# Kernel optimization log

Hardware: AMD Instinct MI355X
Metric: run time of the kernel (lower is better)

The kernel has to match this reference:

```python
import jax, jax.numpy as jnp
import numpy as np

N_NODES = 200000  # num_users + num_items
N_EDGES = 500000
LATENT = 64
N_LAYERS = 3
NEG_SLOPE = 0.01  # F.leaky_relu default
EPS = 1e-16       # PyG geo_softmax denominator epsilon


def setup_inputs() -> dict:
    key = jax.random.key(0)
    k1, k2, k3, k4, k5 = jax.random.split(key, 5)
    edge_index = jax.random.randint(k1, (2, N_EDGES), 0, N_NODES, dtype=jnp.int64 if jax.config.jax_enable_x64 else jnp.int32)
    edge_attrs = jax.random.normal(k2, (N_EDGES, 2), dtype=jnp.float32)
    emb = jax.random.normal(k3, (N_NODES, LATENT), dtype=jnp.float32)
    # per-layer attention params, shape [L, heads=1 -> squeezed, in_channels]
    a_att_w = jax.random.normal(k4, (N_LAYERS, LATENT), dtype=jnp.float32) * 0.1
    r_att_w = jax.random.normal(k5, (N_LAYERS, LATENT), dtype=jnp.float32) * 0.1
    return {"edge_index": edge_index, "edge_attrs": edge_attrs, "emb": emb,
            "a_att_w": a_att_w, "r_att_w": r_att_w}


def _segment_softmax(scores, dst, num_nodes):
    # scores: [E, D] softmax over edges grouped by destination node (PyG geo_softmax)
    m = jax.ops.segment_max(scores, dst, num_segments=num_nodes)  # [N, D]
    m = jnp.where(jnp.isfinite(m), m, 0.0)  # nodes without incoming edges
    w = jnp.exp(scores - m[dst])
    den = jax.ops.segment_sum(w, dst, num_segments=num_nodes)     # [N, D]
    return w / (den[dst] + EPS)


def reference(edge_index, edge_attrs, emb, a_att_w, r_att_w):
    src, dst = edge_index[0], edge_index[1]
    n = emb.shape[0]
    # symmetric degree normalization (degree of destination endpoints)
    deg = jax.ops.segment_sum(jnp.ones_like(dst, dtype=emb.dtype), dst, num_segments=n)
    dinv = jnp.where(deg > 0, deg ** -0.5, 0.0)
    norm = (dinv[src] * dinv[dst])[:, None]  # [E, 1]

    a_e = edge_attrs[:, 0:1]  # [E, 1]
    r_e = edge_attrs[:, 1:2]

    x = emb
    acc = emb  # layer-0 embedding
    for l in range(N_LAYERS):
        scores = (jax.nn.leaky_relu(a_e * a_att_w[l], NEG_SLOPE)
                  + jax.nn.leaky_relu(r_e * r_att_w[l], NEG_SLOPE))  # [E, D]
        attn = _segment_softmax(scores, dst, n)                       # [E, D]
        msg = norm * attn * x[src]                                    # gather + weight
        x = jax.ops.segment_sum(msg, dst, num_segments=n)             # scatter-add
        acc = acc + x
    out = acc / (N_LAYERS + 1)  # mean over layer embeddings
    return out
```

## Files before the change

kernel.cpp:

```cpp
#include <hip/hip_runtime.h>

#define BLK 256
#define LBLK 256
#define CH 1024

__device__ __forceinline__ unsigned short f2bf(float f) {
    unsigned u = __float_as_uint(f);
    u += 0x7FFFu + ((u >> 16) & 1u);
    return (unsigned short)(u >> 16);
}
__device__ __forceinline__ float bf2f(unsigned short h) {
    return __uint_as_float((unsigned)h << 16);
}
__device__ __forceinline__ float4 unpack4(ushort4 h) {
    return make_float4(bf2f(h.x), bf2f(h.y), bf2f(h.z), bf2f(h.w));
}
__device__ __forceinline__ ushort4 pack4(float4 f) {
    ushort4 h; h.x = f2bf(f.x); h.y = f2bf(f.y); h.z = f2bf(f.z); h.w = f2bf(f.w);
    return h;
}


__global__ void k_deg(const int* __restrict__ dst, int* __restrict__ deg,
                      int* __restrict__ rank, int E) {
    int e = blockIdx.x * blockDim.x + threadIdx.x;
    if (e < E) rank[e] = atomicAdd(&deg[dst[e]], 1);
}

__global__ void k_scan1(const int* __restrict__ deg, int* __restrict__ partials, int N) {
    __shared__ int sm[BLK];
    int i0 = blockIdx.x * CH + threadIdx.x * 4;
    int s = 0;
    if (i0 + 3 < N) {
        int4 v = *(const int4*)(deg + i0);
        s = (v.x + v.y) + (v.z + v.w);
    } else {
        for (int k = 0; k < 4; ++k) if (i0 + k < N) s += deg[i0 + k];
    }
    sm[threadIdx.x] = s;
    __syncthreads();
    for (int off = BLK / 2; off > 0; off >>= 1) {
        if (threadIdx.x < off) sm[threadIdx.x] += sm[threadIdx.x + off];
        __syncthreads();
    }
    if (threadIdx.x == 0) partials[blockIdx.x] = sm[0];
}

__global__ void k_scan2(const int* __restrict__ deg, const int* __restrict__ partials,
                        int* __restrict__ row_off, int N, int E, int nb) {
    __shared__ int sp[BLK];
    __shared__ int sm[BLK];
    int b = blockIdx.x, t = threadIdx.x;
    sp[t] = (t < nb) ? partials[t] : 0;
    __syncthreads();
    for (int off = 1; off < BLK; off <<= 1) {
        int add = (t >= off) ? sp[t - off] : 0;
        __syncthreads();
        sp[t] += add;
        __syncthreads();
    }
    int base = (b == 0) ? 0 : sp[b - 1];
    if (b == 0 && t == 0) row_off[N] = E;
    int i0 = b * CH + t * 4;
    int v0 = 0, v1 = 0, v2 = 0, v3 = 0;
    if (i0 + 3 < N) {
        int4 v = *(const int4*)(deg + i0);
        v0 = v.x; v1 = v.y; v2 = v.z; v3 = v.w;
    } else {
        if (i0     < N) v0 = deg[i0];
        if (i0 + 1 < N) v1 = deg[i0 + 1];
        if (i0 + 2 < N) v2 = deg[i0 + 2];
    }
    int tot = (v0 + v1) + (v2 + v3);
    sm[t] = tot;
    __syncthreads();
    for (int off = 1; off < BLK; off <<= 1) {
        int add = (t >= off) ? sm[t - off] : 0;
        __syncthreads();
        sm[t] += add;
        __syncthreads();
    }
    int excl = base + sm[t] - tot;
    int4 r;
    r.x = excl;
    r.y = excl + v0;
    r.z = excl + v0 + v1;
    r.w = excl + v0 + v1 + v2;
    if (i0 + 3 < N) {
        *(int4*)(row_off + i0) = r;
    } else {
        if (i0     < N) row_off[i0]     = r.x;
        if (i0 + 1 < N) row_off[i0 + 1] = r.y;
        if (i0 + 2 < N) row_off[i0 + 2] = r.z;
    }
}

__global__ void k_convfill(const int* __restrict__ src, const int* __restrict__ dst,
                           const float2* __restrict__ attrs, const int* __restrict__ row_off,
                           const int* __restrict__ rank, const int* __restrict__ deg,
                           uint2* __restrict__ csr, const float4* __restrict__ emb4,
                           ushort4* __restrict__ embs, int E, int N16, int gF) {
    int b = blockIdx.x;
    if (b < gF) {
        int e = b * BLK + threadIdx.x;
        if (e >= E) return;
        int pos = row_off[dst[e]] + rank[e];
        float2 ar = attrs[e];
        csr[pos] = make_uint2((unsigned)src[e],
                              (unsigned)f2bf(ar.x) | ((unsigned)f2bf(ar.y) << 16));
    } else {
        int i = (b - gF) * BLK + threadIdx.x;
        if (i >= N16) return;
        int d = deg[i >> 4];
        float dinv = (d > 0) ? rsqrtf((float)d) : 0.0f;
        float4 e = emb4[i];
        embs[i] = pack4(make_float4(dinv * e.x, dinv * e.y, dinv * e.z, dinv * e.w));
    }
}


__device__ __forceinline__ float lrelu(float x) { return fmaxf(x, 0.01f * x); }

__device__ __forceinline__ float4 edge_w4(unsigned ar, const float4& aw, const float4& rw) {
    float a = bf2f((unsigned short)(ar & 0xffffu));
    float r = bf2f((unsigned short)(ar >> 16));
    float4 w;
    w.x = __expf(lrelu(a * aw.x) + lrelu(r * rw.x));
    w.y = __expf(lrelu(a * aw.y) + lrelu(r * rw.y));
    w.z = __expf(lrelu(a * aw.z) + lrelu(r * rw.z));
    w.w = __expf(lrelu(a * aw.w) + lrelu(r * rw.w));
    return w;
}

__device__ __forceinline__ void acc4(float4& num, float4& den,
                                     const float4& w, const ushort4& h, float g) {
    float4 x = unpack4(h);
    den.x += g * w.x; den.y += g * w.y; den.z += g * w.z; den.w += g * w.w;
    num.x += g * w.x * x.x;
    num.y += g * w.y * x.y;
    num.z += g * w.z * x.z;
    num.w += g * w.w * x.w;
}

template<int MODE>
__global__ __launch_bounds__(LBLK) void k_layer(
    const ushort4* __restrict__ xs, const uint2* __restrict__ csr,
    const int* __restrict__ row_off,
    const float4* __restrict__ aw4, const float4* __restrict__ rw4,
    const float4* __restrict__ emb4,
    const ushort4* __restrict__ xsA, const ushort4* __restrict__ xsB,
    ushort4* __restrict__ xsout, float4* __restrict__ out4, int N) {
    const int t = threadIdx.x;
    const int d4 = t & 15;
    const int v = blockIdx.x * (LBLK / 16) + (t >> 4);
    if (v >= N) return;
    const float4 aw = aw4[d4];
    const float4 rw = rw4[d4];
    const int s0 = row_off[v];
    const int s1 = row_off[v + 1];
    const int dv = s1 - s0;
    float4 num = {0.f, 0.f, 0.f, 0.f};
    float4 den = {0.f, 0.f, 0.f, 0.f};
    for (int i = s0; i < s1; i += 4) {
        const int last = s1 - 1;
        uint2 e0 = csr[i];
        uint2 e1 = csr[min(i + 1, last)];
        uint2 e2 = csr[min(i + 2, last)];
        uint2 e3 = csr[min(i + 3, last)];
        ushort4 h0 = xs[(size_t)e0.x * 16 + d4];
        ushort4 h1 = xs[(size_t)e1.x * 16 + d4];
        ushort4 h2 = xs[(size_t)e2.x * 16 + d4];
        ushort4 h3 = xs[(size_t)e3.x * 16 + d4];
        float4 w0 = edge_w4(e0.y, aw, rw);
        float4 w1 = edge_w4(e1.y, aw, rw);
        float4 w2 = edge_w4(e2.y, aw, rw);
        float4 w3 = edge_w4(e3.y, aw, rw);
        float g1 = (i + 1 < s1) ? 1.0f : 0.0f;
        float g2 = (i + 2 < s1) ? 1.0f : 0.0f;
        float g3 = (i + 3 < s1) ? 1.0f : 0.0f;
        acc4(num, den, w0, h0, 1.0f);
        acc4(num, den, w1, h1, g1);
        acc4(num, den, w2, h2, g2);
        acc4(num, den, w3, h3, g3);
    }
    float4 xr;
    xr.x = num.x / (den.x + 1e-16f);
    xr.y = num.y / (den.y + 1e-16f);
    xr.z = num.z / (den.z + 1e-16f);
    xr.w = num.w / (den.w + 1e-16f);
    const float dinv = (dv > 0) ? rsqrtf((float)dv) : 0.0f;
    const size_t o = (size_t)v * 16 + d4;
    if (MODE == 2) {
        const float sd = (dv > 0) ? sqrtf((float)dv) : 0.0f;
        float4 e = emb4[o];
        float4 A = unpack4(xsA[o]);
        float4 B = unpack4(xsB[o]);
        float4 r;
        r.x = (e.x + sd * (A.x + B.x) + dinv * xr.x) * 0.25f;
        r.y = (e.y + sd * (A.y + B.y) + dinv * xr.y) * 0.25f;
        r.z = (e.z + sd * (A.z + B.z) + dinv * xr.z) * 0.25f;
        r.w = (e.w + sd * (A.w + B.w) + dinv * xr.w) * 0.25f;
        out4[o] = r;
    } else {
        const float s = dinv * dinv;
        xsout[o] = pack4(make_float4(s * xr.x, s * xr.y, s * xr.z, s * xr.w));
    }
}


extern "C" void kernel_launch(void* const* d_in, const int* in_sizes, int n_in,
                              void* d_out, int out_size, void* d_ws, size_t ws_size,
                              hipStream_t stream) {
    const int*   ei    = (const int*)d_in[0];
    const float* attrs = (const float*)d_in[1];
    const float* emb   = (const float*)d_in[2];
    const float* a_att = (const float*)d_in[3];
    const float* r_att = (const float*)d_in[4];

    const int E = in_sizes[0] / 2;
    const int N = in_sizes[2] / 64;
    const int* src = ei;
    const int* dst = ei + E;

    char* ws = (char*)d_ws;
    size_t off = 0;
    auto alloc = [&](size_t bytes) {
        void* p = ws + off;
        off += (bytes + 255) & ~(size_t)255;
        return p;
    };
    int*     deg      = (int*)alloc((size_t)N * 4);
    int*     rank     = (int*)alloc((size_t)E * 4);
    int*     row_off  = (int*)alloc((size_t)(N + 1) * 4);
    int*     partials = (int*)alloc((size_t)BLK * 4);
    uint2*   csr      = (uint2*)alloc((size_t)E * 8);
    ushort4* embs     = (ushort4*)alloc((size_t)N * 16 * 8);
    ushort4* xsA      = (ushort4*)alloc((size_t)N * 16 * 8);
    ushort4* xsB      = (ushort4*)alloc((size_t)N * 16 * 8);
    float4*  out      = (float4*)d_out;

    hipMemsetAsync(deg, 0, (size_t)N * 4, stream);

    int gE = (E + BLK - 1) / BLK;
    int nb = (N + CH - 1) / CH;
    int gF = gE;
    int gC = (N * 16 + BLK - 1) / BLK;

    k_deg     <<<gE, BLK, 0, stream>>>(dst, deg, rank, E);
    k_scan1   <<<nb, BLK, 0, stream>>>(deg, partials, N);
    k_scan2   <<<nb, BLK, 0, stream>>>(deg, partials, row_off, N, E, nb);
    k_convfill<<<gF + gC, BLK, 0, stream>>>(src, dst, (const float2*)attrs, row_off,
                                            rank, deg, csr, (const float4*)emb,
                                            embs, E, N * 16, gF);

    const float4* emb4 = (const float4*)emb;
    const float4* aw4  = (const float4*)a_att;
    const float4* rw4  = (const float4*)r_att;

    int gL = (N + (LBLK / 16) - 1) / (LBLK / 16);
    k_layer<0><<<gL, LBLK, 0, stream>>>(embs, csr, row_off, aw4,      rw4,
                                        nullptr, nullptr, nullptr, xsA, nullptr, N);
    k_layer<1><<<gL, LBLK, 0, stream>>>(xsA,  csr, row_off, aw4 + 16, rw4 + 16,
                                        nullptr, nullptr, nullptr, xsB, nullptr, N);
    k_layer<2><<<gL, LBLK, 0, stream>>>(xsB,  csr, row_off, aw4 + 32, rw4 + 32,
                                        emb4, xsA, xsB, nullptr, out, N);
}
```

Measured before the change: 239.3 us.

## Add per-node first-four-edge table to break the row_off to CSR dependency chain

The fill kernel also writes each node's first four edge records into a fixed-stride table, zeroed by an extra memset. The layer kernel reads that table directly by node id, so it can issue the first four neighbour gathers at once instead of waiting for row_off and then the CSR loads. Edges 5 to 8 are prefetched early and the MODE 2 epilogue loads are hoisted. This costs an extra 6.4MB table write plus a memset, and more registers.

```diff
diff --git a/kernel.cpp b/kernel.cpp
--- a/kernel.cpp
+++ b/kernel.cpp
@@ -98,21 +98,25 @@
 __global__ void k_convfill(const int* __restrict__ src, const int* __restrict__ dst,
                            const float2* __restrict__ attrs, const int* __restrict__ row_off,
                            const int* __restrict__ rank, const int* __restrict__ deg,
-                           uint2* __restrict__ csr, const float4* __restrict__ emb4,
+                           uint2* __restrict__ csr, uint2* __restrict__ f4,
+                           const float4* __restrict__ emb4,
                            ushort4* __restrict__ embs, int E, int N16, int gF) {
     int b = blockIdx.x;
     if (b < gF) {
         int e = b * BLK + threadIdx.x;
         if (e >= E) return;
-        int pos = row_off[dst[e]] + rank[e];
+        int d  = dst[e];
+        int rk = rank[e];
         float2 ar = attrs[e];
-        csr[pos] = make_uint2((unsigned)src[e],
-                              (unsigned)f2bf(ar.x) | ((unsigned)f2bf(ar.y) << 16));
+        uint2 rec = make_uint2((unsigned)src[e],
+                               (unsigned)f2bf(ar.x) | ((unsigned)f2bf(ar.y) << 16));
+        csr[row_off[d] + rk] = rec;
+        if (rk < 4) f4[(size_t)d * 4 + rk] = rec;
     } else {
         int i = (b - gF) * BLK + threadIdx.x;
         if (i >= N16) return;
-        int d = deg[i >> 4];
-        float dinv = (d > 0) ? rsqrtf((float)d) : 0.0f;
+        int dg = deg[i >> 4];
+        float dinv = (dg > 0) ? rsqrtf((float)dg) : 0.0f;
         float4 e = emb4[i];
         embs[i] = pack4(make_float4(dinv * e.x, dinv * e.y, dinv * e.z, dinv * e.w));
     }
@@ -145,7 +149,7 @@
 template<int MODE>
 __global__ __launch_bounds__(LBLK) void k_layer(
     const ushort4* __restrict__ xs, const uint2* __restrict__ csr,
-    const int* __restrict__ row_off,
+    const uint2* __restrict__ f4, const int* __restrict__ row_off,
     const float4* __restrict__ aw4, const float4* __restrict__ rw4,
     const float4* __restrict__ emb4,
     const ushort4* __restrict__ xsA, const ushort4* __restrict__ xsB,
@@ -154,52 +158,121 @@
     const int d4 = t & 15;
     const int v = blockIdx.x * (LBLK / 16) + (t >> 4);
     if (v >= N) return;
+    const unsigned nm1 = (unsigned)(N - 1);
+    const size_t o = (size_t)v * 16 + d4;
+
     const float4 aw = aw4[d4];
     const float4 rw = rw4[d4];
+
+    const uint4 fa = *(const uint4*)(f4 + (size_t)v * 4);
+    const uint4 fb = *(const uint4*)(f4 + (size_t)v * 4 + 2);
     const int s0 = row_off[v];
     const int s1 = row_off[v + 1];
-    const int dv = s1 - s0;
+
+    float4 emb_v = {0,0,0,0}, Av = {0,0,0,0}, Bv = {0,0,0,0};
+    if (MODE == 2) {
+        emb_v = emb4[o];
+        Av = unpack4(xsA[o]);
+        Bv = unpack4(xsB[o]);
+    }
+
+    ushort4 h0 = xs[(size_t)min(fa.x, nm1) * 16 + d4];
+    ushort4 h1 = xs[(size_t)min(fa.z, nm1) * 16 + d4];
+    ushort4 h2 = xs[(size_t)min(fb.x, nm1) * 16 + d4];
+    ushort4 h3 = xs[(size_t)min(fb.z, nm1) * 16 + d4];
+
     float4 num = {0.f, 0.f, 0.f, 0.f};
     float4 den = {0.f, 0.f, 0.f, 0.f};
-    for (int i = s0; i < s1; i += 4) {
-        const int last = s1 - 1;
-        uint2 e0 = csr[i];
-        uint2 e1 = csr[min(i + 1, last)];
-        uint2 e2 = csr[min(i + 2, last)];
-        uint2 e3 = csr[min(i + 3, last)];
-        ushort4 h0 = xs[(size_t)e0.x * 16 + d4];
-        ushort4 h1 = xs[(size_t)e1.x * 16 + d4];
-        ushort4 h2 = xs[(size_t)e2.x * 16 + d4];
-        ushort4 h3 = xs[(size_t)e3.x * 16 + d4];
-        float4 w0 = edge_w4(e0.y, aw, rw);
-        float4 w1 = edge_w4(e1.y, aw, rw);
-        float4 w2 = edge_w4(e2.y, aw, rw);
-        float4 w3 = edge_w4(e3.y, aw, rw);
-        float g1 = (i + 1 < s1) ? 1.0f : 0.0f;
-        float g2 = (i + 2 < s1) ? 1.0f : 0.0f;
-        float g3 = (i + 3 < s1) ? 1.0f : 0.0f;
-        acc4(num, den, w0, h0, 1.0f);
+
+    if (s0 + 4 < s1) {
+        const int l = max(s1 - 1, 0);
+        uint2 e4 = csr[min(s0 + 4, l)];
+        uint2 e5 = csr[min(s0 + 5, l)];
+        uint2 e6 = csr[min(s0 + 6, l)];
+        uint2 e7 = csr[min(s0 + 7, l)];
+        ushort4 h4 = xs[(size_t)min(e4.x, nm1) * 16 + d4];
+        ushort4 h5 = xs[(size_t)min(e5.x, nm1) * 16 + d4];
+        ushort4 h6 = xs[(size_t)min(e6.x, nm1) * 16 + d4];
+        ushort4 h7 = xs[(size_t)min(e7.x, nm1) * 16 + d4];
+        {
+            const float g0 = (s0     < s1) ? 1.0f : 0.0f;
+            const float g1 = (s0 + 1 < s1) ? 1.0f : 0.0f;
+            const float g2 = (s0 + 2 < s1) ? 1.0f : 0.0f;
+            const float g3 = (s0 + 3 < s1) ? 1.0f : 0.0f;
+            float4 w0 = edge_w4(fa.y, aw, rw);
+            float4 w1 = edge_w4(fa.w, aw, rw);
+            float4 w2 = edge_w4(fb.y, aw, rw);
+            float4 w3 = edge_w4(fb.w, aw, rw);
+            acc4(num, den, w0, h0, g0);
+            acc4(num, den, w1, h1, g1);
+            acc4(num, den, w2, h2, g2);
+            acc4(num, den, w3, h3, g3);
+        }
+        {
+            const float g4 = (s0 + 4 < s1) ? 1.0f : 0.0f;
+            const float g5 = (s0 + 5 < s1) ? 1.0f : 0.0f;
+            const float g6 = (s0 + 6 < s1) ? 1.0f : 0.0f;
+            const float g7 = (s0 + 7 < s1) ? 1.0f : 0.0f;
+            float4 w4 = edge_w4(e4.y, aw, rw);
+            float4 w5 = edge_w4(e5.y, aw, rw);
+            float4 w6 = edge_w4(e6.y, aw, rw);
+            float4 w7 = edge_w4(e7.y, aw, rw);
+            acc4(num, den, w4, h4, g4);
+            acc4(num, den, w5, h5, g5);
+            acc4(num, den, w6, h6, g6);
+            acc4(num, den, w7, h7, g7);
+        }
+        for (int i = s0 + 8; i < s1; i += 4) {
+            const int last = s1 - 1;
+            uint2 e0 = csr[i];
+            uint2 e1 = csr[min(i + 1, last)];
+            uint2 e2 = csr[min(i + 2, last)];
+            uint2 e3 = csr[min(i + 3, last)];
+            ushort4 t0 = xs[(size_t)e0.x * 16 + d4];
+            ushort4 t1 = xs[(size_t)e1.x * 16 + d4];
+            ushort4 t2 = xs[(size_t)e2.x * 16 + d4];
+            ushort4 t3 = xs[(size_t)e3.x * 16 + d4];
+            float4 w0 = edge_w4(e0.y, aw, rw);
+            float4 w1 = edge_w4(e1.y, aw, rw);
+            float4 w2 = edge_w4(e2.y, aw, rw);
+            float4 w3 = edge_w4(e3.y, aw, rw);
+            float g1 = (i + 1 < s1) ? 1.0f : 0.0f;
+            float g2 = (i + 2 < s1) ? 1.0f : 0.0f;
+            float g3 = (i + 3 < s1) ? 1.0f : 0.0f;
+            acc4(num, den, w0, t0, 1.0f);
+            acc4(num, den, w1, t1, g1);
+            acc4(num, den, w2, t2, g2);
+            acc4(num, den, w3, t3, g3);
+        }
+    } else {
+        const float g0 = (s0     < s1) ? 1.0f : 0.0f;
+        const float g1 = (s0 + 1 < s1) ? 1.0f : 0.0f;
+        const float g2 = (s0 + 2 < s1) ? 1.0f : 0.0f;
+        const float g3 = (s0 + 3 < s1) ? 1.0f : 0.0f;
+        float4 w0 = edge_w4(fa.y, aw, rw);
+        float4 w1 = edge_w4(fa.w, aw, rw);
+        float4 w2 = edge_w4(fb.y, aw, rw);
+        float4 w3 = edge_w4(fb.w, aw, rw);
+        acc4(num, den, w0, h0, g0);
         acc4(num, den, w1, h1, g1);
         acc4(num, den, w2, h2, g2);
         acc4(num, den, w3, h3, g3);
     }
+
     float4 xr;
     xr.x = num.x / (den.x + 1e-16f);
     xr.y = num.y / (den.y + 1e-16f);
     xr.z = num.z / (den.z + 1e-16f);
     xr.w = num.w / (den.w + 1e-16f);
+    const int dv = s1 - s0;
     const float dinv = (dv > 0) ? rsqrtf((float)dv) : 0.0f;
-    const size_t o = (size_t)v * 16 + d4;
     if (MODE == 2) {
         const float sd = (dv > 0) ? sqrtf((float)dv) : 0.0f;
-        float4 e = emb4[o];
-        float4 A = unpack4(xsA[o]);
-        float4 B = unpack4(xsB[o]);
         float4 r;
-        r.x = (e.x + sd * (A.x + B.x) + dinv * xr.x) * 0.25f;
-        r.y = (e.y + sd * (A.y + B.y) + dinv * xr.y) * 0.25f;
-        r.z = (e.z + sd * (A.z + B.z) + dinv * xr.z) * 0.25f;
-        r.w = (e.w + sd * (A.w + B.w) + dinv * xr.w) * 0.25f;
+        r.x = (emb_v.x + sd * (Av.x + Bv.x) + dinv * xr.x) * 0.25f;
+        r.y = (emb_v.y + sd * (Av.y + Bv.y) + dinv * xr.y) * 0.25f;
+        r.z = (emb_v.z + sd * (Av.z + Bv.z) + dinv * xr.z) * 0.25f;
+        r.w = (emb_v.w + sd * (Av.w + Bv.w) + dinv * xr.w) * 0.25f;
         out4[o] = r;
     } else {
         const float s = dinv * dinv;
@@ -234,12 +307,14 @@
     int*     row_off  = (int*)alloc((size_t)(N + 1) * 4);
     int*     partials = (int*)alloc((size_t)BLK * 4);
     uint2*   csr      = (uint2*)alloc((size_t)E * 8);
+    uint2*   f4tab    = (uint2*)alloc((size_t)N * 4 * 8);
     ushort4* embs     = (ushort4*)alloc((size_t)N * 16 * 8);
     ushort4* xsA      = (ushort4*)alloc((size_t)N * 16 * 8);
     ushort4* xsB      = (ushort4*)alloc((size_t)N * 16 * 8);
     float4*  out      = (float4*)d_out;
 
     hipMemsetAsync(deg, 0, (size_t)N * 4, stream);
+    hipMemsetAsync(f4tab, 0, (size_t)N * 4 * 8, stream);
 
     int gE = (E + BLK - 1) / BLK;
     int nb = (N + CH - 1) / CH;
@@ -250,7 +325,7 @@
     k_scan1   <<<nb, BLK, 0, stream>>>(deg, partials, N);
     k_scan2   <<<nb, BLK, 0, stream>>>(deg, partials, row_off, N, E, nb);
     k_convfill<<<gF + gC, BLK, 0, stream>>>(src, dst, (const float2*)attrs, row_off,
-                                            rank, deg, csr, (const float4*)emb,
+                                            rank, deg, csr, f4tab, (const float4*)emb,
                                             embs, E, N * 16, gF);
 
     const float4* emb4 = (const float4*)emb;
@@ -258,10 +333,10 @@
     const float4* rw4  = (const float4*)r_att;
 
     int gL = (N + (LBLK / 16) - 1) / (LBLK / 16);
-    k_layer<0><<<gL, LBLK, 0, stream>>>(embs, csr, row_off, aw4,      rw4,
+    k_layer<0><<<gL, LBLK, 0, stream>>>(embs, csr, f4tab, row_off, aw4,      rw4,
                                         nullptr, nullptr, nullptr, xsA, nullptr, N);
-    k_layer<1><<<gL, LBLK, 0, stream>>>(xsA,  csr, row_off, aw4 + 16, rw4 + 16,
+    k_layer<1><<<gL, LBLK, 0, stream>>>(xsA,  csr, f4tab, row_off, aw4 + 16, rw4 + 16,
                                         nullptr, nullptr, nullptr, xsB, nullptr, N);
-    k_layer<2><<<gL, LBLK, 0, stream>>>(xsB,  csr, row_off, aw4 + 32, rw4 + 32,
+    k_layer<2><<<gL, LBLK, 0, stream>>>(xsB,  csr, f4tab, row_off, aw4 + 32, rw4 + 32,
                                         emb4, xsA, xsB, nullptr, out, N);
 }
```

Measured after the change: 279.9 us. 16.9% more time.
